# Kernel optimization log

Hardware: AMD Instinct MI355X
Metric: run time of the kernel (lower is better)

## Reference

```python
import jax, jax.numpy as jnp
import numpy as np

TH = 1.0  # LIF threshold
EPS = 1e-5  # LayerNorm eps

# Heaviside spike with snntorch ATan surrogate gradient (alpha=2.0)
@jax.custom_vjp
def spike(u):
    return (u > 0).astype(u.dtype)

def _spike_fwd(u):
    return spike(u), u

def _spike_bwd(u, g):
    alpha = 2.0
    return (g * (alpha / 2.0) / (1.0 + (jnp.pi / 2.0 * alpha * u) ** 2),)

spike.defvjp(_spike_fwd, _spike_bwd)


def setup_inputs() -> dict:
    key = jax.random.key(0)
    ks = jax.random.split(key, 8)
    T, B, D_in, H1, H2, D_lat = 200, 256, 256, 512, 512, 128
    spike_input = jax.random.uniform(ks[0], (T, B, D_in), dtype=jnp.float32)
    s1 = 1.0 / np.sqrt(D_in)
    s2 = 1.0 / np.sqrt(H1)
    s3 = 1.0 / np.sqrt(H2)
    return {
        "spike_input": spike_input,
        "W1": jax.random.uniform(ks[1], (H1, D_in), jnp.float32, -s1, s1),
        "b1": jnp.zeros((H1,), jnp.float32),
        "beta0": jnp.float32(0.5),
        "W2": jax.random.uniform(ks[2], (H2, H1), jnp.float32, -s2, s2),
        "b2": jnp.zeros((H2,), jnp.float32),
        "beta1": jnp.float32(0.5),
        "Wout": jax.random.uniform(ks[3], (D_lat, H2), jnp.float32, -s3, s3),
        "bout": jnp.zeros((D_lat,), jnp.float32),
        "ln_gamma": jnp.ones((D_lat,), jnp.float32),
        "ln_beta": jnp.zeros((D_lat,), jnp.float32),
    }


def reference(spike_input, W1, b1, beta0, W2, b2, beta1, Wout, bout, ln_gamma, ln_beta):
    T, B, _ = spike_input.shape
    H1, H2 = W1.shape[0], W2.shape[0]
    be0 = jnp.clip(beta0, 0.0, 1.0)
    be1 = jnp.clip(beta1, 0.0, 1.0)

    def step(carry, x_t):
        m0, m1 = carry
        # layer 0: Linear + Leaky (reset-by-subtraction, reset detached)
        h = x_t @ W1.T + b1
        r0 = jax.lax.stop_gradient((m0 > TH).astype(h.dtype))
        m0 = be0 * m0 + h - r0 * TH
        s0 = spike(m0 - TH)
        # layer 1
        h2 = s0 @ W2.T + b2
        r1 = jax.lax.stop_gradient((m1 > TH).astype(h2.dtype))
        m1 = be1 * m1 + h2 - r1 * TH
        s1 = spike(m1 - TH)
        return (m0, m1), (s0, s1)

    init = (jnp.zeros((B, H1), spike_input.dtype), jnp.zeros((B, H2), spike_input.dtype))
    _, (spk0, spk1) = jax.lax.scan(step, init, spike_input)  # [T,B,H]

    # source appends only the final-timestep activation to hidden_acc
    hidden_mean = spk1[-1]  # [B, H2]
    latent = hidden_mean @ Wout.T + bout
    mu = jnp.mean(latent, axis=-1, keepdims=True)
    var = jnp.var(latent, axis=-1, keepdims=True)
    latent = (latent - mu) * jax.lax.rsqrt(var + EPS) * ln_gamma + ln_beta

    fr0 = jnp.mean(spk0, axis=0)
    fr1 = jnp.mean(spk1, axis=0)
    return latent, fr0, fr1
```

## Files before the change

### kernel.cpp

```cpp
#include <hip/hip_runtime.h>

typedef _Float16 half8 __attribute__((ext_vector_type(8)));
typedef _Float16 half4v __attribute__((ext_vector_type(4)));
typedef float f32x4 __attribute__((ext_vector_type(4)));

#define BATCH 256
#define D_IN 256
#define H1N 512
#define H2N 512
#define D_LAT 128
#define MROWS 51200
#define BHE 131072
#define SC_LO 4.8828125e-4f

__device__ __forceinline__ void glds16(const _Float16* g, _Float16* l) {
    __builtin_amdgcn_global_load_lds(
        (const __attribute__((address_space(1))) unsigned int*)g,
        (__attribute__((address_space(3))) unsigned int*)l, 16, 0, 0);
}

__global__ __launch_bounds__(256) void splitk(const float* __restrict__ in,
                                              _Float16* __restrict__ hi,
                                              _Float16* __restrict__ lo, int n4) {
    int i = blockIdx.x * 256 + threadIdx.x;
    if (i >= n4) return;
    float4 v = reinterpret_cast<const float4*>(in)[i];
    float vv[4] = {v.x, v.y, v.z, v.w};
    half4v h, l;
#pragma unroll
    for (int c = 0; c < 4; ++c) {
        _Float16 hh = (_Float16)vv[c];
        h[c] = hh;
        l[c] = (_Float16)((vv[c] - (float)hh) * 2048.0f);
    }
    reinterpret_cast<half4v*>(hi)[i] = h;
    reinterpret_cast<half4v*>(lo)[i] = l;
}

__device__ __forceinline__ void decode_mn(int d, int& m0, int& n0) {
    const int xcd = d & 7, j = d >> 3;
    const int nt = j & 3, mloc = j >> 2;
    m0 = (mloc * 8 + xcd) * 128;
    n0 = nt * 128;
}

__global__ __launch_bounds__(256, 2) void gemm1_k(const _Float16* __restrict__ Ah,
                                                  const _Float16* __restrict__ Al,
                                                  const _Float16* __restrict__ Bh,
                                                  const _Float16* __restrict__ Bl,
                                                  const float* __restrict__ bias,
                                                  float* __restrict__ C) {
    __shared__ _Float16 sAh[2][128 * 32];
    __shared__ _Float16 sAl[2][128 * 32];
    __shared__ _Float16 sBh[2][128 * 32];
    __shared__ _Float16 sBl[2][128 * 32];

    const int tid = threadIdx.x, lane = tid & 63, wid = tid >> 6;
    int m0, n0;
    decode_mn(blockIdx.x, m0, n0);
    const int wr = wid >> 1, wc = wid & 1;
    const int frow = lane & 15, kb = lane >> 4;
    const int rl = lane >> 2;
    const int lane_off = rl * D_IN + 8 * ((lane & 3) ^ ((rl >> 1) & 3));

    f32x4 acc0[4][4] = {};
    f32x4 acc1[4][4] = {};

    auto stage = [&](int ph, int k0) {
#pragma unroll
        for (int i = 0; i < 8; ++i) {
            const int c = wid + 4 * i;
            const _Float16* gp;
            _Float16* lp;
            if (c < 8)       { gp = Ah + (size_t)(m0 + c * 16) * D_IN;        lp = &sAh[ph][c * 16 * 32]; }
            else if (c < 16) { gp = Al + (size_t)(m0 + (c - 8) * 16) * D_IN;  lp = &sAl[ph][(c - 8) * 16 * 32]; }
            else if (c < 24) { gp = Bh + (size_t)(n0 + (c - 16) * 16) * D_IN; lp = &sBh[ph][(c - 16) * 16 * 32]; }
            else             { gp = Bl + (size_t)(n0 + (c - 24) * 16) * D_IN; lp = &sBl[ph][(c - 24) * 16 * 32]; }
            glds16(gp + k0 + lane_off, lp);
        }
    };

    stage(0, 0);
    __syncthreads();

    for (int kt = 0; kt < D_IN / 32; ++kt) {
        const int ph = kt & 1;
        if (kt < D_IN / 32 - 1) stage(ph ^ 1, (kt + 1) * 32);

        half8 bh[4], bl[4];
#pragma unroll
        for (int ni = 0; ni < 4; ++ni) {
            const int br = wc * 64 + ni * 16 + frow;
            const int off = br * 32 + 8 * (kb ^ ((br >> 1) & 3));
            bh[ni] = *reinterpret_cast<const half8*>(&sBh[ph][off]);
            bl[ni] = *reinterpret_cast<const half8*>(&sBl[ph][off]);
        }
#pragma unroll
        for (int mi = 0; mi < 4; ++mi) {
            const int ar = wr * 64 + mi * 16 + frow;
            const int aoff = ar * 32 + 8 * (kb ^ ((ar >> 1) & 3));
            half8 ah = *reinterpret_cast<const half8*>(&sAh[ph][aoff]);
            half8 al = *reinterpret_cast<const half8*>(&sAl[ph][aoff]);
#pragma unroll
            for (int ni = 0; ni < 4; ++ni) {
                acc0[mi][ni] = __builtin_amdgcn_mfma_f32_16x16x32_f16(ah, bh[ni], acc0[mi][ni], 0, 0, 0);
                acc1[mi][ni] = __builtin_amdgcn_mfma_f32_16x16x32_f16(ah, bl[ni], acc1[mi][ni], 0, 0, 0);
                acc1[mi][ni] = __builtin_amdgcn_mfma_f32_16x16x32_f16(al, bh[ni], acc1[mi][ni], 0, 0, 0);
            }
        }
        __syncthreads();
    }

#pragma unroll
    for (int mi = 0; mi < 4; ++mi)
#pragma unroll
        for (int ni = 0; ni < 4; ++ni) {
            const int col = n0 + wc * 64 + ni * 16 + frow;
            const float bb = bias[col];
#pragma unroll
            for (int r = 0; r < 4; ++r) {
                const int m = m0 + wr * 64 + mi * 16 + kb * 4 + r;
                C[(size_t)m * H1N + col] = acc0[mi][ni][r] + SC_LO * acc1[mi][ni][r] + bb;
            }
        }
}

__global__ __launch_bounds__(256, 2) void gemm2_k(const _Float16* __restrict__ A,
                                                  const _Float16* __restrict__ Bh,
                                                  const _Float16* __restrict__ Bl,
                                                  const float* __restrict__ bias,
                                                  float* __restrict__ C) {
    __shared__ _Float16 sA[2][128 * 32];
    __shared__ _Float16 sBh[2][128 * 32];
    __shared__ _Float16 sBl[2][128 * 32];

    const int tid = threadIdx.x, lane = tid & 63, wid = tid >> 6;
    int m0, n0;
    decode_mn(blockIdx.x, m0, n0);
    const int wr = wid >> 1, wc = wid & 1;
    const int frow = lane & 15, kb = lane >> 4;
    const int rl = lane >> 2;
    const int lane_off = rl * H1N + 8 * ((lane & 3) ^ ((rl >> 1) & 3));

    f32x4 acc0[4][4] = {};
    f32x4 acc1[4][4] = {};

    auto stage = [&](int ph, int k0) {
#pragma unroll
        for (int i = 0; i < 6; ++i) {
            const int c = wid + 4 * i;
            const _Float16* gp;
            _Float16* lp;
            if (c < 8)       { gp = A  + (size_t)(m0 + c * 16) * H1N;         lp = &sA[ph][c * 16 * 32]; }
            else if (c < 16) { gp = Bh + (size_t)(n0 + (c - 8) * 16) * H1N;   lp = &sBh[ph][(c - 8) * 16 * 32]; }
            else             { gp = Bl + (size_t)(n0 + (c - 16) * 16) * H1N;  lp = &sBl[ph][(c - 16) * 16 * 32]; }
            glds16(gp + k0 + lane_off, lp);
        }
    };

    stage(0, 0);
    __syncthreads();

    for (int kt = 0; kt < H1N / 32; ++kt) {
        const int ph = kt & 1;
        if (kt < H1N / 32 - 1) stage(ph ^ 1, (kt + 1) * 32);

        half8 bh[4], bl[4];
#pragma unroll
        for (int ni = 0; ni < 4; ++ni) {
            const int br = wc * 64 + ni * 16 + frow;
            const int off = br * 32 + 8 * (kb ^ ((br >> 1) & 3));
            bh[ni] = *reinterpret_cast<const half8*>(&sBh[ph][off]);
            bl[ni] = *reinterpret_cast<const half8*>(&sBl[ph][off]);
        }
#pragma unroll
        for (int mi = 0; mi < 4; ++mi) {
            const int ar = wr * 64 + mi * 16 + frow;
            half8 a = *reinterpret_cast<const half8*>(&sA[ph][ar * 32 + 8 * (kb ^ ((ar >> 1) & 3))]);
#pragma unroll
            for (int ni = 0; ni < 4; ++ni) {
                acc0[mi][ni] = __builtin_amdgcn_mfma_f32_16x16x32_f16(a, bh[ni], acc0[mi][ni], 0, 0, 0);
                acc1[mi][ni] = __builtin_amdgcn_mfma_f32_16x16x32_f16(a, bl[ni], acc1[mi][ni], 0, 0, 0);
            }
        }
        __syncthreads();
    }

#pragma unroll
    for (int mi = 0; mi < 4; ++mi)
#pragma unroll
        for (int ni = 0; ni < 4; ++ni) {
            const int col = n0 + wc * 64 + ni * 16 + frow;
            const float bb = bias[col];
#pragma unroll
            for (int r = 0; r < 4; ++r) {
                const int m = m0 + wr * 64 + mi * 16 + kb * 4 + r;
                C[(size_t)m * H2N + col] = acc0[mi][ni][r] + SC_LO * acc1[mi][ni][r] + bb;
            }
        }
}

__global__ __launch_bounds__(256) void lif1(const float* __restrict__ H,
                                            const float* __restrict__ beta_ptr,
                                            _Float16* __restrict__ S,
                                            float* __restrict__ fr,
                                            unsigned char* __restrict__ slast,
                                            int writeS, int writeLast) {
    const int idx = blockIdx.x * 256 + threadIdx.x;
    const float be = fminf(fmaxf(beta_ptr[0], 0.f), 1.f);
    float m = 0.f, r = 0.f, c = 0.f;
#pragma unroll 20
    for (int t = 0; t < 200; ++t) {
        const float h = H[(size_t)t * BHE + idx];
        m = be * m + h - r;
        r = (m > 1.0f) ? 1.f : 0.f;
        c += r;
        if (writeS) S[(size_t)t * BHE + idx] = (_Float16)r;
    }
    fr[idx] = c * (1.f / 200.f);
    if (writeLast) slast[idx] = (r > 0.5f) ? 1 : 0;
}

__global__ __launch_bounds__(128) void latent_ln(const unsigned char* __restrict__ s_last,
                                                 const float* __restrict__ Wout,
                                                 const float* __restrict__ bout,
                                                 const float* __restrict__ gamma,
                                                 const float* __restrict__ lbeta,
                                                 float* __restrict__ out) {
    const int b = blockIdx.x;
    const int d = threadIdx.x;
    __shared__ float sv[H2N];
    for (int k = d; k < H2N; k += 128) sv[k] = (float)s_last[b * H2N + k];
    __syncthreads();

    float a = 0.f;
    const float* w = &Wout[(size_t)d * H2N];
#pragma unroll 8
    for (int k = 0; k < H2N; ++k) a = fmaf(sv[k], w[k], a);
    a += bout[d];

    __shared__ float red[128];
    red[d] = a;
    __syncthreads();
    for (int s = 64; s > 0; s >>= 1) {
        if (d < s) red[d] += red[d + s];
        __syncthreads();
    }
    const float mu = red[0] * (1.0f / 128.0f);
    __syncthreads();
    const float df = a - mu;
    red[d] = df * df;
    __syncthreads();
    for (int s = 64; s > 0; s >>= 1) {
        if (d < s) red[d] += red[d + s];
        __syncthreads();
    }
    const float var = red[0] * (1.0f / 128.0f);
    out[(size_t)b * D_LAT + d] = df * (1.0f / sqrtf(var + 1e-5f)) * gamma[d] + lbeta[d];
}

extern "C" void kernel_launch(void* const* d_in, const int* in_sizes, int n_in,
                              void* d_out, int out_size, void* d_ws, size_t ws_size,
                              hipStream_t stream) {
    const float* X     = (const float*)d_in[0];
    const float* W1    = (const float*)d_in[1];
    const float* b1    = (const float*)d_in[2];
    const float* beta0 = (const float*)d_in[3];
    const float* W2    = (const float*)d_in[4];
    const float* b2    = (const float*)d_in[5];
    const float* beta1 = (const float*)d_in[6];
    const float* Wout  = (const float*)d_in[7];
    const float* bout  = (const float*)d_in[8];
    const float* lng   = (const float*)d_in[9];
    const float* lnb   = (const float*)d_in[10];

    float* out    = (float*)d_out;
    float* latent = out;
    float* fr0    = out + BATCH * D_LAT;
    float* fr1    = fr0 + BATCH * H1N;

    char* p = (char*)d_ws;
    float*     H   = (float*)p;              p += (size_t)MROWS * H1N * 4;
    _Float16*  S0  = (_Float16*)p;           p += (size_t)MROWS * H1N * 2;
    _Float16*  Xh  = (_Float16*)p;           p += (size_t)MROWS * D_IN * 2;
    _Float16*  Xl  = (_Float16*)p;           p += (size_t)MROWS * D_IN * 2;
    _Float16*  W1h = (_Float16*)p;           p += (size_t)H1N * D_IN * 2;
    _Float16*  W1l = (_Float16*)p;           p += (size_t)H1N * D_IN * 2;
    _Float16*  W2h = (_Float16*)p;           p += (size_t)H2N * H1N * 2;
    _Float16*  W2l = (_Float16*)p;           p += (size_t)H2N * H1N * 2;
    unsigned char* s1l = (unsigned char*)p;  p += (size_t)BHE;

    splitk<<<dim3(MROWS * D_IN / 4 / 256), 256, 0, stream>>>(X, Xh, Xl, MROWS * D_IN / 4);
    splitk<<<dim3(H1N * D_IN / 4 / 256), 256, 0, stream>>>(W1, W1h, W1l, H1N * D_IN / 4);
    splitk<<<dim3(H2N * H1N / 4 / 256), 256, 0, stream>>>(W2, W2h, W2l, H2N * H1N / 4);

    gemm1_k<<<dim3((MROWS / 128) * (H1N / 128)), 256, 0, stream>>>(Xh, Xl, W1h, W1l, b1, H);
    lif1<<<dim3(BHE / 256), 256, 0, stream>>>(H, beta0, S0, fr0, nullptr, 1, 0);
    gemm2_k<<<dim3((MROWS / 128) * (H2N / 128)), 256, 0, stream>>>(S0, W2h, W2l, b2, H);
    lif1<<<dim3(BHE / 256), 256, 0, stream>>>(H, beta1, nullptr, fr1, s1l, 0, 1);
    latent_ln<<<dim3(BATCH), 128, 0, stream>>>(s1l, Wout, bout, lng, lnb, latent);
}
```

Before: 382.6 us.

## Fold split-precision terms into extended-K GEMMs with 256x128 triple-buffered tiles

New measurement: 328.8 us. 1.16x faster.

```diff
diff --git a/kernel.cpp b/kernel.cpp
--- a/kernel.cpp
+++ b/kernel.cpp
@@ -19,12 +19,31 @@
         (__attribute__((address_space(3))) unsigned int*)l, 16, 0, 0);
 }
 
-__global__ __launch_bounds__(256) void splitk(const float* __restrict__ in,
-                                              _Float16* __restrict__ hi,
-                                              _Float16* __restrict__ lo, int n4) {
+__global__ __launch_bounds__(256) void splitX(const float* __restrict__ X,
+                                              _Float16* __restrict__ A1) {
     int i = blockIdx.x * 256 + threadIdx.x;
-    if (i >= n4) return;
-    float4 v = reinterpret_cast<const float4*>(in)[i];
+    int m = i >> 6, kq = i & 63;
+    float4 v = reinterpret_cast<const float4*>(X)[i];
+    float vv[4] = {v.x, v.y, v.z, v.w};
+    half4v h, hs, d;
+#pragma unroll
+    for (int c = 0; c < 4; ++c) {
+        _Float16 hh = (_Float16)vv[c];
+        h[c] = hh;
+        hs[c] = (_Float16)((float)hh * SC_LO);
+        d[c] = (_Float16)(vv[c] - (float)hh);
+    }
+    size_t base = (size_t)m * 768 + kq * 4;
+    *reinterpret_cast<half4v*>(&A1[base]) = h;
+    *reinterpret_cast<half4v*>(&A1[base + 256]) = hs;
+    *reinterpret_cast<half4v*>(&A1[base + 512]) = d;
+}
+
+__global__ __launch_bounds__(256) void splitW1(const float* __restrict__ W,
+                                               _Float16* __restrict__ Bp) {
+    int i = blockIdx.x * 256 + threadIdx.x;
+    int r = i >> 6, kq = i & 63;
+    float4 v = reinterpret_cast<const float4*>(W)[i];
     float vv[4] = {v.x, v.y, v.z, v.w};
     half4v h, l;
 #pragma unroll
@@ -33,82 +52,123 @@
         h[c] = hh;
         l[c] = (_Float16)((vv[c] - (float)hh) * 2048.0f);
     }
-    reinterpret_cast<half4v*>(hi)[i] = h;
-    reinterpret_cast<half4v*>(lo)[i] = l;
-}
-
-__device__ __forceinline__ void decode_mn(int d, int& m0, int& n0) {
-    const int xcd = d & 7, j = d >> 3;
+    size_t base = (size_t)r * 768 + kq * 4;
+    *reinterpret_cast<half4v*>(&Bp[base]) = h;
+    *reinterpret_cast<half4v*>(&Bp[base + 256]) = l;
+    *reinterpret_cast<half4v*>(&Bp[base + 512]) = h;
+}
+
+__global__ __launch_bounds__(256) void splitW2(const float* __restrict__ W,
+                                               _Float16* __restrict__ Bp) {
+    int i = blockIdx.x * 256 + threadIdx.x;
+    int r = i >> 7, kq = i & 127;
+    float4 v = reinterpret_cast<const float4*>(W)[i];
+    float vv[4] = {v.x, v.y, v.z, v.w};
+    half4v h, l;
+#pragma unroll
+    for (int c = 0; c < 4; ++c) {
+        _Float16 hh = (_Float16)vv[c];
+        h[c] = hh;
+        l[c] = (_Float16)((vv[c] - (float)hh) * 2048.0f);
+    }
+    size_t base = (size_t)r * 1024 + kq * 4;
+    *reinterpret_cast<half4v*>(&Bp[base]) = h;
+    *reinterpret_cast<half4v*>(&Bp[base + 512]) = l;
+}
+
+template <int KT>
+__global__ __launch_bounds__(512, 1) void gemm8(const _Float16* __restrict__ A,
+                                                const _Float16* __restrict__ B,
+                                                const float* __restrict__ bias,
+                                                float* __restrict__ C) {
+    constexpr int K = KT * 64;
+    __shared__ _Float16 sA[3][256 * 64];
+    __shared__ _Float16 sB[3][128 * 64];
+
+    const int tid = threadIdx.x, lane = tid & 63, wid = tid >> 6;
+    const int bid = blockIdx.x;
+    const int xcd = bid & 7, j = bid >> 3;
     const int nt = j & 3, mloc = j >> 2;
-    m0 = (mloc * 8 + xcd) * 128;
-    n0 = nt * 128;
-}
-
-__global__ __launch_bounds__(256, 2) void gemm1_k(const _Float16* __restrict__ Ah,
-                                                  const _Float16* __restrict__ Al,
-                                                  const _Float16* __restrict__ Bh,
-                                                  const _Float16* __restrict__ Bl,
-                                                  const float* __restrict__ bias,
-                                                  float* __restrict__ C) {
-    __shared__ _Float16 sAh[2][128 * 32];
-    __shared__ _Float16 sAl[2][128 * 32];
-    __shared__ _Float16 sBh[2][128 * 32];
-    __shared__ _Float16 sBl[2][128 * 32];
-
-    const int tid = threadIdx.x, lane = tid & 63, wid = tid >> 6;
-    int m0, n0;
-    decode_mn(blockIdx.x, m0, n0);
-    const int wr = wid >> 1, wc = wid & 1;
+    const int m0 = (mloc * 8 + xcd) * 256, n0 = nt * 128;
+
+    const int wr = wid & 3, wc = wid >> 2;
     const int frow = lane & 15, kb = lane >> 4;
-    const int rl = lane >> 2;
-    const int lane_off = rl * D_IN + 8 * ((lane & 3) ^ ((rl >> 1) & 3));
-
-    f32x4 acc0[4][4] = {};
-    f32x4 acc1[4][4] = {};
-
-    auto stage = [&](int ph, int k0) {
-#pragma unroll
-        for (int i = 0; i < 8; ++i) {
-            const int c = wid + 4 * i;
-            const _Float16* gp;
-            _Float16* lp;
-            if (c < 8)       { gp = Ah + (size_t)(m0 + c * 16) * D_IN;        lp = &sAh[ph][c * 16 * 32]; }
-            else if (c < 16) { gp = Al + (size_t)(m0 + (c - 8) * 16) * D_IN;  lp = &sAl[ph][(c - 8) * 16 * 32]; }
-            else if (c < 24) { gp = Bh + (size_t)(n0 + (c - 16) * 16) * D_IN; lp = &sBh[ph][(c - 16) * 16 * 32]; }
-            else             { gp = Bl + (size_t)(n0 + (c - 24) * 16) * D_IN; lp = &sBl[ph][(c - 24) * 16 * 32]; }
-            glds16(gp + k0 + lane_off, lp);
+
+    const int lr = lane >> 3, ls = lane & 7;
+    const int sl = 8 * (ls ^ lr);
+
+    const _Float16* ga0 = A + (size_t)(m0 + (wid)*8 + lr) * K + sl;
+    const _Float16* ga1 = A + (size_t)(m0 + (wid + 8) * 8 + lr) * K + sl;
+    const _Float16* ga2 = A + (size_t)(m0 + (wid + 16) * 8 + lr) * K + sl;
+    const _Float16* ga3 = A + (size_t)(m0 + (wid + 24) * 8 + lr) * K + sl;
+    const _Float16* gb0 = B + (size_t)(n0 + (wid)*8 + lr) * K + sl;
+    const _Float16* gb1 = B + (size_t)(n0 + (wid + 8) * 8 + lr) * K + sl;
+    const int da0 = wid * 512, da1 = (wid + 8) * 512, da2 = (wid + 16) * 512, da3 = (wid + 24) * 512;
+    const int db0 = wid * 512, db1 = (wid + 8) * 512;
+
+    const int f7 = frow & 7;
+    const int sk0 = 8 * (kb ^ f7);
+    const int sk1 = 8 * ((4 + kb) ^ f7);
+    const int abase = (wr * 64 + frow) * 64;
+    const int bbase = (wc * 64 + frow) * 64;
+
+    f32x4 acc[4][4] = {};
+
+    glds16(ga0, &sA[0][da0]); glds16(ga1, &sA[0][da1]); glds16(ga2, &sA[0][da2]);
+    glds16(ga3, &sA[0][da3]); glds16(gb0, &sB[0][db0]); glds16(gb1, &sB[0][db1]);
+    glds16(ga0 + 64, &sA[1][da0]); glds16(ga1 + 64, &sA[1][da1]); glds16(ga2 + 64, &sA[1][da2]);
+    glds16(ga3 + 64, &sA[1][da3]); glds16(gb0 + 64, &sB[1][db0]); glds16(gb1 + 64, &sB[1][db1]);
+    asm volatile("s_waitcnt vmcnt(6)" ::: "memory");
+    __builtin_amdgcn_s_barrier();
+
+#pragma unroll
+    for (int t = 0; t < KT; ++t) {
+        const int cur = t % 3, nx2 = (t + 2) % 3;
+        const int ko = (t + 2) * 64;
+        half8 av[4], bv[4];
+#pragma unroll
+        for (int mi = 0; mi < 4; ++mi)
+            av[mi] = *reinterpret_cast<const half8*>(&sA[cur][abase + mi * 1024 + sk0]);
+#pragma unroll
+        for (int ni = 0; ni < 4; ++ni)
+            bv[ni] = *reinterpret_cast<const half8*>(&sB[cur][bbase + ni * 1024 + sk0]);
+        if (t + 2 < KT) {
+            glds16(ga0 + ko, &sA[nx2][da0]);
+            glds16(ga1 + ko, &sA[nx2][da1]);
+            glds16(ga2 + ko, &sA[nx2][da2]);
         }
-    };
-
-    stage(0, 0);
-    __syncthreads();
-
-    for (int kt = 0; kt < D_IN / 32; ++kt) {
-        const int ph = kt & 1;
-        if (kt < D_IN / 32 - 1) stage(ph ^ 1, (kt + 1) * 32);
-
-        half8 bh[4], bl[4];
-#pragma unroll
-        for (int ni = 0; ni < 4; ++ni) {
-            const int br = wc * 64 + ni * 16 + frow;
-            const int off = br * 32 + 8 * (kb ^ ((br >> 1) & 3));
-            bh[ni] = *reinterpret_cast<const half8*>(&sBh[ph][off]);
-            bl[ni] = *reinterpret_cast<const half8*>(&sBl[ph][off]);
+        __builtin_amdgcn_s_barrier();
+        __builtin_amdgcn_s_setprio(1);
+#pragma unroll
+        for (int mi = 0; mi < 4; ++mi)
+#pragma unroll
+            for (int ni = 0; ni < 4; ++ni)
+                acc[mi][ni] = __builtin_amdgcn_mfma_f32_16x16x32_f16(av[mi], bv[ni], acc[mi][ni], 0, 0, 0);
+        __builtin_amdgcn_s_setprio(0);
+        __builtin_amdgcn_s_barrier();
+#pragma unroll
+        for (int mi = 0; mi < 4; ++mi)
+            av[mi] = *reinterpret_cast<const half8*>(&sA[cur][abase + mi * 1024 + sk1]);
+#pragma unroll
+        for (int ni = 0; ni < 4; ++ni)
+            bv[ni] = *reinterpret_cast<const half8*>(&sB[cur][bbase + ni * 1024 + sk1]);
+        if (t + 2 < KT) {
+            glds16(ga3 + ko, &sA[nx2][da3]);
+            glds16(gb0 + ko, &sB[nx2][db0]);
+            glds16(gb1 + ko, &sB[nx2][db1]);
+            asm volatile("s_waitcnt vmcnt(6)" ::: "memory");
+        } else if (t + 1 < KT) {
+            asm volatile("s_waitcnt vmcnt(0)" ::: "memory");
         }
-#pragma unroll
-        for (int mi = 0; mi < 4; ++mi) {
-            const int ar = wr * 64 + mi * 16 + frow;
-            const int aoff = ar * 32 + 8 * (kb ^ ((ar >> 1) & 3));
-            half8 ah = *reinterpret_cast<const half8*>(&sAh[ph][aoff]);
-            half8 al = *reinterpret_cast<const half8*>(&sAl[ph][aoff]);
-#pragma unroll
-            for (int ni = 0; ni < 4; ++ni) {
-                acc0[mi][ni] = __builtin_amdgcn_mfma_f32_16x16x32_f16(ah, bh[ni], acc0[mi][ni], 0, 0, 0);
-                acc1[mi][ni] = __builtin_amdgcn_mfma_f32_16x16x32_f16(ah, bl[ni], acc1[mi][ni], 0, 0, 0);
-                acc1[mi][ni] = __builtin_amdgcn_mfma_f32_16x16x32_f16(al, bh[ni], acc1[mi][ni], 0, 0, 0);
-            }
-        }
-        __syncthreads();
+        __builtin_amdgcn_s_barrier();
+        __builtin_amdgcn_s_setprio(1);
+#pragma unroll
+        for (int mi = 0; mi < 4; ++mi)
+#pragma unroll
+            for (int ni = 0; ni < 4; ++ni)
+                acc[mi][ni] = __builtin_amdgcn_mfma_f32_16x16x32_f16(av[mi], bv[ni], acc[mi][ni], 0, 0, 0);
+        __builtin_amdgcn_s_setprio(0);
+        __builtin_amdgcn_s_barrier();
     }
 
 #pragma unroll
@@ -120,92 +180,36 @@
 #pragma unroll
             for (int r = 0; r < 4; ++r) {
                 const int m = m0 + wr * 64 + mi * 16 + kb * 4 + r;
-                C[(size_t)m * H1N + col] = acc0[mi][ni][r] + SC_LO * acc1[mi][ni][r] + bb;
+                C[(size_t)m * 512 + col] = acc[mi][ni][r] + bb;
             }
         }
 }
 
-__global__ __launch_bounds__(256, 2) void gemm2_k(const _Float16* __restrict__ A,
-                                                  const _Float16* __restrict__ Bh,
-                                                  const _Float16* __restrict__ Bl,
-                                                  const float* __restrict__ bias,
-                                                  float* __restrict__ C) {
-    __shared__ _Float16 sA[2][128 * 32];
-    __shared__ _Float16 sBh[2][128 * 32];
-    __shared__ _Float16 sBl[2][128 * 32];
-
-    const int tid = threadIdx.x, lane = tid & 63, wid = tid >> 6;
-    int m0, n0;
-    decode_mn(blockIdx.x, m0, n0);
-    const int wr = wid >> 1, wc = wid & 1;
-    const int frow = lane & 15, kb = lane >> 4;
-    const int rl = lane >> 2;
-    const int lane_off = rl * H1N + 8 * ((lane & 3) ^ ((rl >> 1) & 3));
-
-    f32x4 acc0[4][4] = {};
-    f32x4 acc1[4][4] = {};
-
-    auto stage = [&](int ph, int k0) {
-#pragma unroll
-        for (int i = 0; i < 6; ++i) {
-            const int c = wid + 4 * i;
-            const _Float16* gp;
-            _Float16* lp;
-            if (c < 8)       { gp = A  + (size_t)(m0 + c * 16) * H1N;         lp = &sA[ph][c * 16 * 32]; }
-            else if (c < 16) { gp = Bh + (size_t)(n0 + (c - 8) * 16) * H1N;   lp = &sBh[ph][(c - 8) * 16 * 32]; }
-            else             { gp = Bl + (size_t)(n0 + (c - 16) * 16) * H1N;  lp = &sBl[ph][(c - 16) * 16 * 32]; }
-            glds16(gp + k0 + lane_off, lp);
-        }
-    };
-
-    stage(0, 0);
-    __syncthreads();
-
-    for (int kt = 0; kt < H1N / 32; ++kt) {
-        const int ph = kt & 1;
-        if (kt < H1N / 32 - 1) stage(ph ^ 1, (kt + 1) * 32);
-
-        half8 bh[4], bl[4];
-#pragma unroll
-        for (int ni = 0; ni < 4; ++ni) {
-            const int br = wc * 64 + ni * 16 + frow;
-            const int off = br * 32 + 8 * (kb ^ ((br >> 1) & 3));
-            bh[ni] = *reinterpret_cast<const half8*>(&sBh[ph][off]);
-            bl[ni] = *reinterpret_cast<const half8*>(&sBl[ph][off]);
-        }
-#pragma unroll
-        for (int mi = 0; mi < 4; ++mi) {
-            const int ar = wr * 64 + mi * 16 + frow;
-            half8 a = *reinterpret_cast<const half8*>(&sA[ph][ar * 32 + 8 * (kb ^ ((ar >> 1) & 3))]);
-#pragma unroll
-            for (int ni = 0; ni < 4; ++ni) {
-                acc0[mi][ni] = __builtin_amdgcn_mfma_f32_16x16x32_f16(a, bh[ni], acc0[mi][ni], 0, 0, 0);
-                acc1[mi][ni] = __builtin_amdgcn_mfma_f32_16x16x32_f16(a, bl[ni], acc1[mi][ni], 0, 0, 0);
-            }
-        }
-        __syncthreads();
-    }
-
-#pragma unroll
-    for (int mi = 0; mi < 4; ++mi)
-#pragma unroll
-        for (int ni = 0; ni < 4; ++ni) {
-            const int col = n0 + wc * 64 + ni * 16 + frow;
-            const float bb = bias[col];
-#pragma unroll
-            for (int r = 0; r < 4; ++r) {
-                const int m = m0 + wr * 64 + mi * 16 + kb * 4 + r;
-                C[(size_t)m * H2N + col] = acc0[mi][ni][r] + SC_LO * acc1[mi][ni][r] + bb;
-            }
-        }
-}
-
-__global__ __launch_bounds__(256) void lif1(const float* __restrict__ H,
-                                            const float* __restrict__ beta_ptr,
-                                            _Float16* __restrict__ S,
-                                            float* __restrict__ fr,
-                                            unsigned char* __restrict__ slast,
-                                            int writeS, int writeLast) {
+__global__ __launch_bounds__(256) void lif_s(const float* __restrict__ H,
+                                             const float* __restrict__ beta_ptr,
+                                             _Float16* __restrict__ Sp,
+                                             float* __restrict__ fr) {
+    const int idx = blockIdx.x * 256 + threadIdx.x;
+    const int b = idx >> 9, n = idx & 511;
+    const float be = fminf(fmaxf(beta_ptr[0], 0.f), 1.f);
+    float m = 0.f, r = 0.f, c = 0.f;
+#pragma unroll 8
+    for (int t = 0; t < 200; ++t) {
+        const float h = H[(size_t)t * BHE + idx];
+        m = be * m + h - r;
+        r = (m > 1.0f) ? 1.f : 0.f;
+        c += r;
+        const size_t row = (size_t)(t * 256 + b) * 1024;
+        Sp[row + n] = (_Float16)r;
+        Sp[row + 512 + n] = (_Float16)(r * SC_LO);
+    }
+    fr[idx] = c * (1.f / 200.f);
+}
+
+__global__ __launch_bounds__(256) void lif_f(const float* __restrict__ H,
+                                             const float* __restrict__ beta_ptr,
+                                             float* __restrict__ fr,
+                                             unsigned char* __restrict__ slast) {
     const int idx = blockIdx.x * 256 + threadIdx.x;
     const float be = fminf(fmaxf(beta_ptr[0], 0.f), 1.f);
     float m = 0.f, r = 0.f, c = 0.f;
@@ -215,10 +219,9 @@
         m = be * m + h - r;
         r = (m > 1.0f) ? 1.f : 0.f;
         c += r;
-        if (writeS) S[(size_t)t * BHE + idx] = (_Float16)r;
     }
     fr[idx] = c * (1.f / 200.f);
-    if (writeLast) slast[idx] = (r > 0.5f) ? 1 : 0;
+    slast[idx] = (r > 0.5f) ? 1 : 0;
 }
 
 __global__ __launch_bounds__(128) void latent_ln(const unsigned char* __restrict__ s_last,
@@ -280,23 +283,20 @@
     float* fr1    = fr0 + BATCH * H1N;
 
     char* p = (char*)d_ws;
-    float*     H   = (float*)p;              p += (size_t)MROWS * H1N * 4;
-    _Float16*  S0  = (_Float16*)p;           p += (size_t)MROWS * H1N * 2;
-    _Float16*  Xh  = (_Float16*)p;           p += (size_t)MROWS * D_IN * 2;
-    _Float16*  Xl  = (_Float16*)p;           p += (size_t)MROWS * D_IN * 2;
-    _Float16*  W1h = (_Float16*)p;           p += (size_t)H1N * D_IN * 2;
-    _Float16*  W1l = (_Float16*)p;           p += (size_t)H1N * D_IN * 2;
-    _Float16*  W2h = (_Float16*)p;           p += (size_t)H2N * H1N * 2;
-    _Float16*  W2l = (_Float16*)p;           p += (size_t)H2N * H1N * 2;
+    _Float16* Sp  = (_Float16*)p;            p += (size_t)MROWS * 1024 * 2;
+    float*    H   = (float*)p;               p += (size_t)MROWS * 512 * 4;
+    _Float16* B1p = (_Float16*)p;            p += (size_t)512 * 768 * 2;
+    _Float16* B2p = (_Float16*)p;            p += (size_t)512 * 1024 * 2;
     unsigned char* s1l = (unsigned char*)p;  p += (size_t)BHE;
-
-    splitk<<<dim3(MROWS * D_IN / 4 / 256), 256, 0, stream>>>(X, Xh, Xl, MROWS * D_IN / 4);
-    splitk<<<dim3(H1N * D_IN / 4 / 256), 256, 0, stream>>>(W1, W1h, W1l, H1N * D_IN / 4);
-    splitk<<<dim3(H2N * H1N / 4 / 256), 256, 0, stream>>>(W2, W2h, W2l, H2N * H1N / 4);
-
-    gemm1_k<<<dim3((MROWS / 128) * (H1N / 128)), 256, 0, stream>>>(Xh, Xl, W1h, W1l, b1, H);
-    lif1<<<dim3(BHE / 256), 256, 0, stream>>>(H, beta0, S0, fr0, nullptr, 1, 0);
-    gemm2_k<<<dim3((MROWS / 128) * (H2N / 128)), 256, 0, stream>>>(S0, W2h, W2l, b2, H);
-    lif1<<<dim3(BHE / 256), 256, 0, stream>>>(H, beta1, nullptr, fr1, s1l, 0, 1);
+    _Float16* A1p = Sp;
+
+    splitX<<<dim3(MROWS * 64 / 256), 256, 0, stream>>>(X, A1p);
+    splitW1<<<dim3(512 * 64 / 256), 256, 0, stream>>>(W1, B1p);
+    splitW2<<<dim3(512 * 128 / 256), 256, 0, stream>>>(W2, B2p);
+
+    gemm8<12><<<dim3(800), 512, 0, stream>>>(A1p, B1p, b1, H);
+    lif_s<<<dim3(BHE / 256), 256, 0, stream>>>(H, beta0, Sp, fr0);
+    gemm8<16><<<dim3(800), 512, 0, stream>>>(Sp, B2p, b2, H);
+    lif_f<<<dim3(BHE / 256), 256, 0, stream>>>(H, beta1, fr1, s1l);
     latent_ln<<<dim3(BATCH), 128, 0, stream>>>(s1l, Wout, bout, lng, lnb, latent);
 }
```
